# Kernel tuning notes

Measured on AMD Instinct MI355X. Metric: run time of the kernel, lower is better.

Reference implementation:

```python
import jax, jax.numpy as jnp
import numpy as np

TEMPERATURE = 0.1  # init arg `temperature`


def _l2_normalize(x):
    return x / jnp.sqrt(jnp.sum(x * x, axis=1, keepdims=True))


def setup_inputs() -> dict:
    key = jax.random.key(0)
    k1, k2, k3 = jax.random.split(key, 3)
    B, D, Q = 2048, 128, 65536
    projections_1 = jax.random.normal(k1, (B, D), dtype=jnp.float32)
    projections_2 = jax.random.normal(k2, (B, D), dtype=jnp.float32)
    # queue is initialized row-l2-normalized in the original module
    feature_queue = _l2_normalize(jax.random.normal(k3, (Q, D), dtype=jnp.float32))
    return {"projections_1": projections_1, "projections_2": projections_2,
            "feature_queue": feature_queue}


def reference(projections_1, projections_2, feature_queue):
    # NNCLR.contrastive_loss (per-sample losses), including nearest_neighbour.
    p1 = _l2_normalize(projections_1)  # [B, D]
    p2 = _l2_normalize(projections_2)  # [B, D]

    def nearest_neighbour(p):
        # [B, Q] similarity -> top-1 index -> gather from queue
        sims = jnp.einsum('bd,qd->bq', p, feature_queue)
        idx = jnp.argmax(sims, axis=1)  # [B]
        nn = feature_queue[idx]         # [B, D]
        # straight-through: value = nn, gradient flows to p
        return p + jax.lax.stop_gradient(nn - p)

    nn1 = nearest_neighbour(p1)
    nn2 = nearest_neighbour(p2)

    s_1_2_1 = jnp.einsum('id,jd->ij', nn1, p2) / TEMPERATURE
    s_1_2_2 = jnp.einsum('id,jd->ij', p2, nn1) / TEMPERATURE
    s_2_1_1 = jnp.einsum('id,jd->ij', nn2, p1) / TEMPERATURE
    s_2_1_2 = jnp.einsum('id,jd->ij', p1, nn2) / TEMPERATURE

    logits = jnp.concatenate([s_1_2_1, s_1_2_2, s_2_1_1, s_2_1_2], axis=0)  # [4B, B]
    B = p1.shape[0]
    labels = jnp.tile(jnp.arange(B), 4)  # [4B]
    logp = jax.nn.log_softmax(logits, axis=1)
    loss = -jnp.take_along_axis(logp, labels[:, None], axis=1)[:, 0]  # [4B]
    return loss
```

## Files before the change

### kernel.cpp

```cpp
#include <hip/hip_runtime.h>

#define S 132
#define SCALE 10.0f
#define EPS_MARGIN 0.008f
#define SROWS_CAP 480
#define ROWCHUNK 48

typedef __attribute__((ext_vector_type(8))) short short8;
typedef __attribute__((ext_vector_type(4))) float floatx4;

#define MFMA16(a, b, c) __builtin_amdgcn_mfma_f32_16x16x32_bf16((a), (b), (c), 0, 0, 0)

__device__ __forceinline__ unsigned int ordered_bits(float f) {
    unsigned int b = __float_as_uint(f);
    return (b & 0x80000000u) ? ~b : (b | 0x80000000u);
}
__device__ __forceinline__ float from_ordered(unsigned int u) {
    return __uint_as_float((u & 0x80000000u) ? (u ^ 0x80000000u) : ~u);
}
__device__ __forceinline__ short bf_rne(float x) {
    unsigned int u = __float_as_uint(x);
    return (short)((u + 0x7FFFu + ((u >> 16) & 1u)) >> 16);
}
__device__ __forceinline__ float bf2f(short s) {
    return __uint_as_float(((unsigned int)(unsigned short)s) << 16);
}

__global__ __launch_bounds__(256) void k_prep_qcvt(const float* __restrict__ p1,
                                                   const float* __restrict__ p2,
                                                   const float* __restrict__ queue,
                                                   float* __restrict__ pn,
                                                   short* __restrict__ pnb,
                                                   short* __restrict__ qb,
                                                   unsigned int* __restrict__ mbest,
                                                   unsigned long long* __restrict__ best,
                                                   float* __restrict__ sums) {
    int b = blockIdx.x;
    if (b < 1024) {
        int sub = threadIdx.x >> 6;
        int t = threadIdx.x & 63;
        int row = b * 4 + sub;
        const float* src = (row < 2048) ? (p1 + (size_t)row * 128)
                                        : (p2 + (size_t)(row - 2048) * 128);
        float2 v = ((const float2*)src)[t];
        float ss = v.x * v.x + v.y * v.y;
        #pragma unroll
        for (int o = 32; o; o >>= 1) ss += __shfl_xor(ss, o);
        float inv = 1.0f / sqrtf(ss);
        float2 o2; o2.x = v.x * inv; o2.y = v.y * inv;
        ((float2*)(pn + (size_t)row * 128))[t] = o2;
        unsigned int pk = (unsigned int)(unsigned short)bf_rne(o2.x)
                        | ((unsigned int)(unsigned short)bf_rne(o2.y) << 16);
        ((unsigned int*)(pnb + (size_t)row * 128))[t] = pk;
        if (t == 0) { mbest[row] = 0u; best[row] = 0ULL; }
        if (row < 128) sums[row * 64 + t] = 0.0f;
    } else {
        size_t i = ((size_t)(b - 1024) * 256 + threadIdx.x) * 8;
        float4 f0 = *(const float4*)(queue + i);
        float4 f1 = *(const float4*)(queue + i + 4);
        short8 o;
        o[0] = bf_rne(f0.x); o[1] = bf_rne(f0.y); o[2] = bf_rne(f0.z); o[3] = bf_rne(f0.w);
        o[4] = bf_rne(f1.x); o[5] = bf_rne(f1.y); o[6] = bf_rne(f1.z); o[7] = bf_rne(f1.w);
        *(short8*)(qb + i) = o;
    }
}

__device__ __forceinline__ void screen_tile(const short8 A[8][4],
                                            short8 b0, short8 b1, short8 b2, short8 b3,
                                            float rmax[8][4]) {
    floatx4 acc[8];
    floatx4 zero = {0.0f, 0.0f, 0.0f, 0.0f};
    #pragma unroll
    for (int rf = 0; rf < 8; ++rf) acc[rf] = MFMA16(A[rf][0], b0, zero);
    #pragma unroll
    for (int rf = 0; rf < 8; ++rf) acc[rf] = MFMA16(A[rf][1], b1, acc[rf]);
    #pragma unroll
    for (int rf = 0; rf < 8; ++rf) acc[rf] = MFMA16(A[rf][2], b2, acc[rf]);
    #pragma unroll
    for (int rf = 0; rf < 8; ++rf) acc[rf] = MFMA16(A[rf][3], b3, acc[rf]);
    #pragma unroll
    for (int rf = 0; rf < 8; ++rf)
        #pragma unroll
        for (int r = 0; r < 4; ++r) rmax[rf][r] = fmaxf(rmax[rf][r], acc[rf][r]);
}

__global__ __launch_bounds__(256, 2) void k_screen(const short* __restrict__ pnb,
                                                   const short* __restrict__ qb,
                                                   unsigned int* __restrict__ mbest,
                                                   float* __restrict__ smax) {
    int tid = threadIdx.x;
    int lane = tid & 63, wv = tid >> 6;
    int n16 = lane & 15, quad = lane >> 4;

    int id = blockIdx.x;
    int xcd = id & 7;
    int g = id >> 3;
    int rowblk = g & 7;
    int qsub = g >> 3;
    int qsplit = xcd * 8 + qsub;
    int rowbase = rowblk * 512 + wv * 128;
    int qstart = qsplit * 1024;

    short8 A[8][4];
    #pragma unroll
    for (int rf = 0; rf < 8; ++rf) {
        const short* ap = pnb + (size_t)(rowbase + rf * 16 + n16) * 128 + quad * 8;
        #pragma unroll
        for (int kk = 0; kk < 4; ++kk)
            A[rf][kk] = *(const short8*)(ap + kk * 32);
    }
    #pragma unroll
    for (int rf = 0; rf < 8; ++rf)
        #pragma unroll
        for (int kk = 0; kk < 4; ++kk)
            asm volatile("" : "+v"(A[rf][kk]));

    float rmax[8][4];
    #pragma unroll
    for (int rf = 0; rf < 8; ++rf)
        #pragma unroll
        for (int r = 0; r < 4; ++r) rmax[rf][r] = -1e30f;

    const short* lp = qb + (size_t)(qstart + n16) * 128 + quad * 8;
    short8 a0 = *(const short8*)(lp), a1 = *(const short8*)(lp + 32),
           a2 = *(const short8*)(lp + 64), a3 = *(const short8*)(lp + 96);

    for (int t = 0; t < 64; t += 2) {
        if ((t & 15) == 0) __syncthreads();
        const short* p1p = lp + 2048;
        short8 b0 = *(const short8*)(p1p), b1 = *(const short8*)(p1p + 32),
               b2 = *(const short8*)(p1p + 64), b3 = *(const short8*)(p1p + 96);
        screen_tile(A, a0, a1, a2, a3, rmax);
        const short* p2p = lp + 4096;
        a0 = *(const short8*)(p2p); a1 = *(const short8*)(p2p + 32);
        a2 = *(const short8*)(p2p + 64); a3 = *(const short8*)(p2p + 96);
        screen_tile(A, b0, b1, b2, b3, rmax);
        lp += 4096;
    }

    #pragma unroll
    for (int rf = 0; rf < 8; ++rf)
        #pragma unroll
        for (int r = 0; r < 4; ++r) {
            float v = rmax[rf][r];
            v = fmaxf(v, __shfl_xor(v, 1));
            v = fmaxf(v, __shfl_xor(v, 2));
            v = fmaxf(v, __shfl_xor(v, 4));
            v = fmaxf(v, __shfl_xor(v, 8));
            if (n16 == 0) {
                int row = rowbase + rf * 16 + quad * 4 + r;
                atomicMax(&mbest[row], ordered_bits(v));
                smax[(size_t)qsplit * 4096 + row] = v;
            }
        }
}

__global__ __launch_bounds__(256, 4) void k_rescreen(const short* __restrict__ pnb,
                                                     const short* __restrict__ qb,
                                                     const unsigned int* __restrict__ mbest,
                                                     const float* __restrict__ smax,
                                                     const float* __restrict__ pn,
                                                     const float* __restrict__ queue,
                                                     unsigned long long* __restrict__ best) {
    __shared__ unsigned short rows[SROWS_CAP];
    __shared__ int nsh;
    int b = blockIdx.x;
    int s = b & 63;
    int qp = b >> 6;
    int tid = threadIdx.x;
    if (tid == 0) nsh = 0;
    __syncthreads();
    const float* sm = smax + (size_t)s * 4096;
    #pragma unroll
    for (int j = 0; j < 16; ++j) {
        int row = tid + 256 * j;
        float thr = from_ordered(mbest[row]) - EPS_MARGIN;
        if (sm[row] > thr) {
            int pos = atomicAdd(&nsh, 1);
            if (pos < SROWS_CAP) rows[pos] = (unsigned short)row;
        }
    }
    __syncthreads();
    int n = nsh; if (n > SROWS_CAP) n = SROWS_CAP;
    if (n == 0) return;

    int lane = tid & 63, wv = tid >> 6;
    int n16 = lane & 15, quad = lane >> 4;
    int qt = qp * 4 + wv;
    int qrow = s * 1024 + qt * 16 + n16;

    const short* bp = qb + (size_t)qrow * 128 + quad * 8;
    short8 b0 = *(const short8*)(bp);
    short8 b1 = *(const short8*)(bp + 32);
    short8 b2 = *(const short8*)(bp + 64);
    short8 b3 = *(const short8*)(bp + 96);

    for (int base = 0; base < n; base += ROWCHUNK) {
        short8 Af[3][4]; float th[3][4]; int rowC[3][4];
        #pragma unroll
        for (int rt = 0; rt < 3; ++rt) {
            int ia = base + rt * 16 + n16;
            int rA = rows[ia < n ? ia : base];
            const short* ap = pnb + (size_t)rA * 128 + quad * 8;
            #pragma unroll
            for (int kk = 0; kk < 4; ++kk) Af[rt][kk] = *(const short8*)(ap + kk * 32);
            #pragma unroll
            for (int r = 0; r < 4; ++r) {
                int ic = base + rt * 16 + quad * 4 + r;
                if (ic < n) {
                    int rr = rows[ic];
                    rowC[rt][r] = rr;
                    th[rt][r] = from_ordered(mbest[rr]) - EPS_MARGIN;
                } else { rowC[rt][r] = 0; th[rt][r] = 3.0e38f; }
            }
        }
        #pragma unroll
        for (int rt = 0; rt < 3; ++rt) {
            floatx4 zero = {0.0f, 0.0f, 0.0f, 0.0f};
            floatx4 acc = MFMA16(Af[rt][0], b0, zero);
            acc = MFMA16(Af[rt][1], b1, acc);
            acc = MFMA16(Af[rt][2], b2, acc);
            acc = MFMA16(Af[rt][3], b3, acc);
            #pragma unroll
            for (int r = 0; r < 4; ++r) {
                unsigned long long mb = __ballot(acc[r] > th[rt][r]);
                while (mb) {
                    int L = __builtin_ctzll(mb);
                    mb &= mb - 1;
                    int row = __shfl(rowC[rt][r], L);
                    int q   = __shfl(qrow, L);
                    float2 a  = ((const float2*)(pn + (size_t)row * 128))[lane];
                    float2 bq = ((const float2*)(queue + (size_t)q * 128))[lane];
                    float d = a.x * bq.x + a.y * bq.y;
                    #pragma unroll
                    for (int o = 32; o; o >>= 1) d += __shfl_xor(d, o);
                    if (lane == 0) {
                        unsigned long long pk = ((unsigned long long)ordered_bits(d) << 32)
                                              | (unsigned long long)(unsigned int)(~q);
                        atomicMax(&best[row], pk);
                    }
                }
            }
        }
    }
}

__global__ __launch_bounds__(256) void k_gemm_lse(const unsigned long long* __restrict__ best,
                                                  const float* __restrict__ queue,
                                                  const float* __restrict__ pn,
                                                  float* __restrict__ sums,
                                                  float* __restrict__ dg) {
    __shared__ __align__(16) float al[64 * S];
    __shared__ __align__(16) float bl[64 * S];
    __shared__ float red[64][17];
    int tid = threadIdx.x;
    int z = blockIdx.z;
    const float* B = pn + (z ? 0 : 2048 * 128);
    float* rowsum = sums + z * 4096;
    float* colsum = sums + z * 4096 + 2048;
    float* diag = dg + z * 2048;
    int arow0 = z * 2048 + blockIdx.x * 64;

    #pragma unroll
    for (int i = tid; i < 1024; i += 256) {
        int r = i >> 4, c = (i & 15) * 8;
        unsigned int idx = (~(unsigned int)(best[arow0 + r] & 0xFFFFFFFFull)) & 0xFFFFu;
        const float* qr = queue + (size_t)idx * 128 + c;
        float4 f0 = *(const float4*)(qr);
        float4 f1 = *(const float4*)(qr + 4);
        float* dst = &al[r * S + c];
        dst[0] = bf2f(bf_rne(f0.x)); dst[1] = bf2f(bf_rne(f0.y));
        dst[2] = bf2f(bf_rne(f0.z)); dst[3] = bf2f(bf_rne(f0.w));
        dst[4] = bf2f(bf_rne(f1.x)); dst[5] = bf2f(bf_rne(f1.y));
        dst[6] = bf2f(bf_rne(f1.z)); dst[7] = bf2f(bf_rne(f1.w));
    }
    const float4* bsrc = (const float4*)(B + (size_t)blockIdx.y * 64 * 128);
    #pragma unroll
    for (int i = tid; i < 2048; i += 256) {
        int r = i >> 5, c = i & 31;
        *(float4*)&bl[r * S + c * 4] = bsrc[i];
    }
    __syncthreads();
    int ty = tid >> 4, tx = tid & 15;
    float acc[4][4] = {};
    #pragma unroll 2
    for (int k = 0; k < 128; k += 4) {
        float4 a[4], b[4];
        #pragma unroll
        for (int i = 0; i < 4; ++i) a[i] = *(const float4*)&al[(ty + 16 * i) * S + k];
        #pragma unroll
        for (int j = 0; j < 4; ++j) b[j] = *(const float4*)&bl[(tx + 16 * j) * S + k];
        #pragma unroll
        for (int i = 0; i < 4; ++i)
            #pragma unroll
            for (int j = 0; j < 4; ++j)
                acc[i][j] += a[i].x * b[j].x + a[i].y * b[j].y +
                             a[i].z * b[j].z + a[i].w * b[j].w;
    }
    int rowbase = blockIdx.x * 64, colbase = blockIdx.y * 64;

    float e[4][4], rs[4], cs[4];
    #pragma unroll
    for (int i = 0; i < 4; ++i) { rs[i] = 0.0f; cs[i] = 0.0f; }
    #pragma unroll
    for (int i = 0; i < 4; ++i)
        #pragma unroll
        for (int j = 0; j < 4; ++j) {
            e[i][j] = __expf(acc[i][j] * SCALE - 10.0f);
            rs[i] += e[i][j];
        }
    #pragma unroll
    for (int j = 0; j < 4; ++j)
        #pragma unroll
        for (int i = 0; i < 4; ++i) cs[j] += e[i][j];

    if (rowbase == colbase && ty == tx) {
        #pragma unroll
        for (int i = 0; i < 4; ++i) diag[rowbase + ty + 16 * i] = acc[i][i];
    }

    #pragma unroll
    for (int i = 0; i < 4; ++i) red[ty + 16 * i][tx] = rs[i];
    __syncthreads();
    if (tid < 64) {
        float s = 0.0f;
        #pragma unroll
        for (int x = 0; x < 16; ++x) s += red[tid][x];
        atomicAdd(&rowsum[rowbase + tid], s);
    }
    __syncthreads();
    #pragma unroll
    for (int j = 0; j < 4; ++j) red[tx + 16 * j][ty] = cs[j];
    __syncthreads();
    if (tid < 64) {
        float s = 0.0f;
        #pragma unroll
        for (int x = 0; x < 16; ++x) s += red[tid][x];
        atomicAdd(&colsum[colbase + tid], s);
    }
}

__global__ void k_final(const float* __restrict__ sums,
                        const float* __restrict__ dg1, const float* __restrict__ dg2,
                        float* __restrict__ out) {
    int idx = blockIdx.x * 256 + threadIdx.x;
    int seg = idx >> 11, r = idx & 2047;
    float s = sums[seg * 2048 + r];
    float d = (seg < 2) ? dg1[r] : dg2[r];
    out[idx] = 10.0f + logf(s) - d * SCALE;
}

extern "C" void kernel_launch(void* const* d_in, const int* in_sizes, int n_in,
                              void* d_out, int out_size, void* d_ws, size_t ws_size,
                              hipStream_t stream) {
    const float* p1    = (const float*)d_in[0];
    const float* p2    = (const float*)d_in[1];
    const float* queue = (const float*)d_in[2];
    float* out = (float*)d_out;

    char* w = (char*)d_ws;
    float* pn   = (float*)w;
    float* smax = (float*)(w + (2u << 20));
    short* qb   = (short*)(w + (3u << 20));
    short* pnb  = (short*)(w + (19u << 20));
    char* b2 = w + (20u << 20);
    unsigned int* mbest = (unsigned int*)b2;
    unsigned long long* best = (unsigned long long*)(b2 + (16u << 10));
    float* sums = (float*)(b2 + (48u << 10));
    float* dg1  = sums + 8192;
    float* dg2  = dg1 + 2048;

    k_prep_qcvt<<<5120, 256, 0, stream>>>(p1, p2, queue, pn, pnb, qb, mbest, best, sums);
    k_screen<<<512, 256, 0, stream>>>(pnb, qb, mbest, smax);
    k_rescreen<<<64 * 16, 256, 0, stream>>>(pnb, qb, mbest, smax, pn, queue, best);
    k_gemm_lse<<<dim3(32, 32, 2), 256, 0, stream>>>(best, queue, pn, sums, dg1);
    k_final<<<32, 256, 0, stream>>>(sums, dg1, dg2, out);
}
```

Before: 234.8 us.

## Restructure screen kernel with smaller per-wave row tile and software-pipelined MFMA/max

The screening kernel now runs 512-thread blocks where each wave holds 64 query rows instead of 128, and each block covers a 2048-entry queue slice instead of 1024, halving the number of splits. The inner loop is software-pipelined: the MFMA chain for one tile overlaps with the max-reduction of the previous tile's accumulators and with loading the next B fragments. Rescreen indexing is updated to the 32-split layout. Lower register pressure should raise occupancy, but each wave reuses its queue loads over fewer rows, and rescreen candidate counts per split may grow.

Result: slower. 288.0 us (+22.6%).

```diff
diff --git a/kernel.cpp b/kernel.cpp
--- a/kernel.cpp
+++ b/kernel.cpp
@@ -65,26 +65,30 @@
     }
 }
 
-__device__ __forceinline__ void screen_tile(const short8 A[8][4],
-                                            short8 b0, short8 b1, short8 b2, short8 b3,
-                                            float rmax[8][4]) {
-    floatx4 acc[8];
+__device__ __forceinline__ void loadB4(short8 B[4], const short* p) {
+    #pragma unroll
+    for (int kk = 0; kk < 4; ++kk) B[kk] = *(const short8*)(p + kk * 32);
+}
+__device__ __forceinline__ void chain4(const short8 A[4][4], const short8 B[4],
+                                       floatx4 acc[4]) {
     floatx4 zero = {0.0f, 0.0f, 0.0f, 0.0f};
     #pragma unroll
-    for (int rf = 0; rf < 8; ++rf) acc[rf] = MFMA16(A[rf][0], b0, zero);
-    #pragma unroll
-    for (int rf = 0; rf < 8; ++rf) acc[rf] = MFMA16(A[rf][1], b1, acc[rf]);
-    #pragma unroll
-    for (int rf = 0; rf < 8; ++rf) acc[rf] = MFMA16(A[rf][2], b2, acc[rf]);
-    #pragma unroll
-    for (int rf = 0; rf < 8; ++rf) acc[rf] = MFMA16(A[rf][3], b3, acc[rf]);
-    #pragma unroll
-    for (int rf = 0; rf < 8; ++rf)
+    for (int rf = 0; rf < 4; ++rf) acc[rf] = MFMA16(A[rf][0], B[0], zero);
+    #pragma unroll
+    for (int rf = 0; rf < 4; ++rf) acc[rf] = MFMA16(A[rf][1], B[1], acc[rf]);
+    #pragma unroll
+    for (int rf = 0; rf < 4; ++rf) acc[rf] = MFMA16(A[rf][2], B[2], acc[rf]);
+    #pragma unroll
+    for (int rf = 0; rf < 4; ++rf) acc[rf] = MFMA16(A[rf][3], B[3], acc[rf]);
+}
+__device__ __forceinline__ void fmax4(float rmax[4][4], const floatx4 acc[4]) {
+    #pragma unroll
+    for (int rf = 0; rf < 4; ++rf)
         #pragma unroll
         for (int r = 0; r < 4; ++r) rmax[rf][r] = fmaxf(rmax[rf][r], acc[rf][r]);
 }
 
-__global__ __launch_bounds__(256, 2) void k_screen(const short* __restrict__ pnb,
+__global__ __launch_bounds__(512, 2) void k_screen(const short* __restrict__ pnb,
                                                    const short* __restrict__ qb,
                                                    unsigned int* __restrict__ mbest,
                                                    float* __restrict__ smax) {
@@ -97,49 +101,48 @@
     int g = id >> 3;
     int rowblk = g & 7;
     int qsub = g >> 3;
-    int qsplit = xcd * 8 + qsub;
-    int rowbase = rowblk * 512 + wv * 128;
-    int qstart = qsplit * 1024;
-
-    short8 A[8][4];
-    #pragma unroll
-    for (int rf = 0; rf < 8; ++rf) {
+    int qsplit = xcd * 4 + qsub;
+    int rowbase = rowblk * 512 + wv * 64;
+    int qstart = qsplit * 2048;
+
+    short8 A[4][4];
+    #pragma unroll
+    for (int rf = 0; rf < 4; ++rf) {
         const short* ap = pnb + (size_t)(rowbase + rf * 16 + n16) * 128 + quad * 8;
         #pragma unroll
         for (int kk = 0; kk < 4; ++kk)
             A[rf][kk] = *(const short8*)(ap + kk * 32);
     }
-    #pragma unroll
-    for (int rf = 0; rf < 8; ++rf)
-        #pragma unroll
-        for (int kk = 0; kk < 4; ++kk)
-            asm volatile("" : "+v"(A[rf][kk]));
-
-    float rmax[8][4];
-    #pragma unroll
-    for (int rf = 0; rf < 8; ++rf)
+
+    float rmax[4][4];
+    #pragma unroll
+    for (int rf = 0; rf < 4; ++rf)
         #pragma unroll
         for (int r = 0; r < 4; ++r) rmax[rf][r] = -1e30f;
 
     const short* lp = qb + (size_t)(qstart + n16) * 128 + quad * 8;
-    short8 a0 = *(const short8*)(lp), a1 = *(const short8*)(lp + 32),
-           a2 = *(const short8*)(lp + 64), a3 = *(const short8*)(lp + 96);
-
-    for (int t = 0; t < 64; t += 2) {
-        if ((t & 15) == 0) __syncthreads();
-        const short* p1p = lp + 2048;
-        short8 b0 = *(const short8*)(p1p), b1 = *(const short8*)(p1p + 32),
-               b2 = *(const short8*)(p1p + 64), b3 = *(const short8*)(p1p + 96);
-        screen_tile(A, a0, a1, a2, a3, rmax);
-        const short* p2p = lp + 4096;
-        a0 = *(const short8*)(p2p); a1 = *(const short8*)(p2p + 32);
-        a2 = *(const short8*)(p2p + 64); a3 = *(const short8*)(p2p + 96);
-        screen_tile(A, b0, b1, b2, b3, rmax);
-        lp += 4096;
-    }
-
-    #pragma unroll
-    for (int rf = 0; rf < 8; ++rf)
+    short8 Ba[4], Bb[4];
+    floatx4 accA[4], accB[4];
+
+    loadB4(Ba, lp);
+    chain4(A, Ba, accB);
+    loadB4(Bb, lp + 2048);
+
+    for (int t = 1; t < 127; t += 2) {
+        if (((t - 1) & 15) == 0) __syncthreads();
+        loadB4(Ba, lp + (size_t)(t + 1) * 2048);
+        chain4(A, Bb, accA);
+        fmax4(rmax, accB);
+        loadB4(Bb, lp + (size_t)(t + 2) * 2048);
+        chain4(A, Ba, accB);
+        fmax4(rmax, accA);
+    }
+    chain4(A, Bb, accA);
+    fmax4(rmax, accB);
+    fmax4(rmax, accA);
+
+    #pragma unroll
+    for (int rf = 0; rf < 4; ++rf)
         #pragma unroll
         for (int r = 0; r < 4; ++r) {
             float v = rmax[rf][r];
@@ -165,8 +168,8 @@
     __shared__ unsigned short rows[SROWS_CAP];
     __shared__ int nsh;
     int b = blockIdx.x;
-    int s = b & 63;
-    int qp = b >> 6;
+    int s = b & 31;
+    int qp = b >> 5;
     int tid = threadIdx.x;
     if (tid == 0) nsh = 0;
     __syncthreads();
@@ -187,7 +190,7 @@
     int lane = tid & 63, wv = tid >> 6;
     int n16 = lane & 15, quad = lane >> 4;
     int qt = qp * 4 + wv;
-    int qrow = s * 1024 + qt * 16 + n16;
+    int qrow = s * 2048 + qt * 16 + n16;
 
     const short* bp = qb + (size_t)qrow * 128 + quad * 8;
     short8 b0 = *(const short8*)(bp);
@@ -371,8 +374,8 @@
     float* dg2  = dg1 + 2048;
 
     k_prep_qcvt<<<5120, 256, 0, stream>>>(p1, p2, queue, pn, pnb, qb, mbest, best, sums);
-    k_screen<<<512, 256, 0, stream>>>(pnb, qb, mbest, smax);
-    k_rescreen<<<64 * 16, 256, 0, stream>>>(pnb, qb, mbest, smax, pn, queue, best);
+    k_screen<<<256, 512, 0, stream>>>(pnb, qb, mbest, smax);
+    k_rescreen<<<32 * 32, 256, 0, stream>>>(pnb, qb, mbest, smax, pn, queue, best);
     k_gemm_lse<<<dim3(32, 32, 2), 256, 0, stream>>>(best, queue, pn, sums, dg1);
     k_final<<<32, 256, 0, stream>>>(sums, dg1, dg2, out);
 }
```

## Run the logits GEMM on bf16 MFMA with a hi/lo split of the projections

Applied to the files above, without the earlier changes.

Replaces the fp32 LDS-tiled FMA GEMM in k_gemm_lse with bf16 MFMA 16x16x32 instructions. The normalized projections are split into high and low bf16 parts in the prep kernel to keep near-fp32 accuracy on the B operand, while the nearest-neighbour rows stay bf16-rounded as before. Tiles grow to 128x128 with operands loaded straight into registers instead of through shared memory, and row and column sums are reduced with shuffles. The cost is an extra bf16 buffer written in prep and twice as many MFMAs for the hi/lo passes, but it removes the scalar FMA bottleneck.

Measured after the change: 215.5 us. 1.09x faster.

```diff
diff --git a/kernel.cpp b/kernel.cpp
--- a/kernel.cpp
+++ b/kernel.cpp
@@ -1,6 +1,5 @@
 #include <hip/hip_runtime.h>
 
-#define S 132
 #define SCALE 10.0f
 #define EPS_MARGIN 0.008f
 #define SROWS_CAP 480
@@ -31,6 +30,7 @@
                                                    const float* __restrict__ queue,
                                                    float* __restrict__ pn,
                                                    short* __restrict__ pnb,
+                                                   short* __restrict__ pnl,
                                                    short* __restrict__ qb,
                                                    unsigned int* __restrict__ mbest,
                                                    unsigned long long* __restrict__ best,
@@ -49,9 +49,14 @@
         float inv = 1.0f / sqrtf(ss);
         float2 o2; o2.x = v.x * inv; o2.y = v.y * inv;
         ((float2*)(pn + (size_t)row * 128))[t] = o2;
-        unsigned int pk = (unsigned int)(unsigned short)bf_rne(o2.x)
-                        | ((unsigned int)(unsigned short)bf_rne(o2.y) << 16);
+        short hx = bf_rne(o2.x), hy = bf_rne(o2.y);
+        unsigned int pk = (unsigned int)(unsigned short)hx
+                        | ((unsigned int)(unsigned short)hy << 16);
         ((unsigned int*)(pnb + (size_t)row * 128))[t] = pk;
+        short lx = bf_rne(o2.x - bf2f(hx)), ly = bf_rne(o2.y - bf2f(hy));
+        unsigned int pl = (unsigned int)(unsigned short)lx
+                        | ((unsigned int)(unsigned short)ly << 16);
+        ((unsigned int*)(pnl + (size_t)row * 128))[t] = pl;
         if (t == 0) { mbest[row] = 0u; best[row] = 0ULL; }
         if (row < 128) sums[row * 64 + t] = 0.0f;
     } else {
@@ -245,98 +250,97 @@
     }
 }
 
-__global__ __launch_bounds__(256) void k_gemm_lse(const unsigned long long* __restrict__ best,
-                                                  const float* __restrict__ queue,
-                                                  const float* __restrict__ pn,
-                                                  float* __restrict__ sums,
-                                                  float* __restrict__ dg) {
-    __shared__ __align__(16) float al[64 * S];
-    __shared__ __align__(16) float bl[64 * S];
-    __shared__ float red[64][17];
+__global__ __launch_bounds__(256, 2) void k_gemm_lse(const unsigned long long* __restrict__ best,
+                                                     const float* __restrict__ queue,
+                                                     const short* __restrict__ pnb,
+                                                     const short* __restrict__ pnl,
+                                                     float* __restrict__ sums,
+                                                     float* __restrict__ dg) {
+    __shared__ float red[4][128];
     int tid = threadIdx.x;
-    int z = blockIdx.z;
-    const float* B = pn + (z ? 0 : 2048 * 128);
+    int lane = tid & 63, wv = tid >> 6;
+    int n16 = lane & 15, quad = lane >> 4;
+    int z = blockIdx.z, xb = blockIdx.x, yb = blockIdx.y;
+
+    short8 A[2][4];
+    #pragma unroll
+    for (int rf = 0; rf < 2; ++rf) {
+        int row = z * 2048 + xb * 128 + wv * 32 + rf * 16 + n16;
+        unsigned int idx = (~(unsigned int)(best[row] & 0xFFFFFFFFull)) & 0xFFFFu;
+        const float* qr = queue + (size_t)idx * 128 + quad * 8;
+        #pragma unroll
+        for (int kk = 0; kk < 4; ++kk) {
+            float4 f0 = *(const float4*)(qr + kk * 32);
+            float4 f1 = *(const float4*)(qr + kk * 32 + 4);
+            short8 a;
+            a[0] = bf_rne(f0.x); a[1] = bf_rne(f0.y); a[2] = bf_rne(f0.z); a[3] = bf_rne(f0.w);
+            a[4] = bf_rne(f1.x); a[5] = bf_rne(f1.y); a[6] = bf_rne(f1.z); a[7] = bf_rne(f1.w);
+            A[rf][kk] = a;
+        }
+    }
+
+    int bbase = (z ? 0 : 2048) + yb * 128;
+    const short* bh0 = pnb + (size_t)(bbase + n16) * 128 + quad * 8;
+    const short* bl0 = pnl + (size_t)(bbase + n16) * 128 + quad * 8;
+
+    float rs[2][4] = {};
     float* rowsum = sums + z * 4096;
     float* colsum = sums + z * 4096 + 2048;
-    float* diag = dg + z * 2048;
-    int arow0 = z * 2048 + blockIdx.x * 64;
-
-    #pragma unroll
-    for (int i = tid; i < 1024; i += 256) {
-        int r = i >> 4, c = (i & 15) * 8;
-        unsigned int idx = (~(unsigned int)(best[arow0 + r] & 0xFFFFFFFFull)) & 0xFFFFu;
-        const float* qr = queue + (size_t)idx * 128 + c;
-        float4 f0 = *(const float4*)(qr);
-        float4 f1 = *(const float4*)(qr + 4);
-        float* dst = &al[r * S + c];
-        dst[0] = bf2f(bf_rne(f0.x)); dst[1] = bf2f(bf_rne(f0.y));
-        dst[2] = bf2f(bf_rne(f0.z)); dst[3] = bf2f(bf_rne(f0.w));
-        dst[4] = bf2f(bf_rne(f1.x)); dst[5] = bf2f(bf_rne(f1.y));
-        dst[6] = bf2f(bf_rne(f1.z)); dst[7] = bf2f(bf_rne(f1.w));
-    }
-    const float4* bsrc = (const float4*)(B + (size_t)blockIdx.y * 64 * 128);
-    #pragma unroll
-    for (int i = tid; i < 2048; i += 256) {
-        int r = i >> 5, c = i & 31;
-        *(float4*)&bl[r * S + c * 4] = bsrc[i];
-    }
+
+    #pragma unroll 1
+    for (int ct = 0; ct < 8; ++ct) {
+        const short* ph = bh0 + (size_t)ct * 16 * 128;
+        const short* pl = bl0 + (size_t)ct * 16 * 128;
+        short8 h0 = *(const short8*)(ph),      h1 = *(const short8*)(ph + 32),
+               h2 = *(const short8*)(ph + 64), h3 = *(const short8*)(ph + 96);
+        short8 l0 = *(const short8*)(pl),      l1 = *(const short8*)(pl + 32),
+               l2 = *(const short8*)(pl + 64), l3 = *(const short8*)(pl + 96);
+        floatx4 acc0, acc1;
+        floatx4 zero = {0.0f, 0.0f, 0.0f, 0.0f};
+        acc0 = MFMA16(A[0][0], h0, zero); acc1 = MFMA16(A[1][0], h0, zero);
+        acc0 = MFMA16(A[0][1], h1, acc0); acc1 = MFMA16(A[1][1], h1, acc1);
+        acc0 = MFMA16(A[0][2], h2, acc0); acc1 = MFMA16(A[1][2], h2, acc1);
+        acc0 = MFMA16(A[0][3], h3, acc0); acc1 = MFMA16(A[1][3], h3, acc1);
+        acc0 = MFMA16(A[0][0], l0, acc0); acc1 = MFMA16(A[1][0], l0, acc1);
+        acc0 = MFMA16(A[0][1], l1, acc0); acc1 = MFMA16(A[1][1], l1, acc1);
+        acc0 = MFMA16(A[0][2], l2, acc0); acc1 = MFMA16(A[1][2], l2, acc1);
+        acc0 = MFMA16(A[0][3], l3, acc0); acc1 = MFMA16(A[1][3], l3, acc1);
+
+        float csv = 0.0f;
+        #pragma unroll
+        for (int rf = 0; rf < 2; ++rf)
+            #pragma unroll
+            for (int r = 0; r < 4; ++r) {
+                float a = rf ? acc1[r] : acc0[r];
+                int row_l = wv * 32 + rf * 16 + quad * 4 + r;
+                if (xb == yb && row_l == ct * 16 + n16)
+                    dg[z * 2048 + xb * 128 + row_l] = a;
+                float e = __expf(a * SCALE - 10.0f);
+                rs[rf][r] += e;
+                csv += e;
+            }
+        csv += __shfl_xor(csv, 16);
+        csv += __shfl_xor(csv, 32);
+        if (quad == 0) red[wv][ct * 16 + n16] = csv;
+    }
+
+    #pragma unroll
+    for (int rf = 0; rf < 2; ++rf)
+        #pragma unroll
+        for (int r = 0; r < 4; ++r) {
+            float v = rs[rf][r];
+            v += __shfl_xor(v, 1);
+            v += __shfl_xor(v, 2);
+            v += __shfl_xor(v, 4);
+            v += __shfl_xor(v, 8);
+            if (n16 == 0)
+                atomicAdd(&rowsum[xb * 128 + wv * 32 + rf * 16 + quad * 4 + r], v);
+        }
+
     __syncthreads();
-    int ty = tid >> 4, tx = tid & 15;
-    float acc[4][4] = {};
-    #pragma unroll 2
-    for (int k = 0; k < 128; k += 4) {
-        float4 a[4], b[4];
-        #pragma unroll
-        for (int i = 0; i < 4; ++i) a[i] = *(const float4*)&al[(ty + 16 * i) * S + k];
-        #pragma unroll
-        for (int j = 0; j < 4; ++j) b[j] = *(const float4*)&bl[(tx + 16 * j) * S + k];
-        #pragma unroll
-        for (int i = 0; i < 4; ++i)
-            #pragma unroll
-            for (int j = 0; j < 4; ++j)
-                acc[i][j] += a[i].x * b[j].x + a[i].y * b[j].y +
-                             a[i].z * b[j].z + a[i].w * b[j].w;
-    }
-    int rowbase = blockIdx.x * 64, colbase = blockIdx.y * 64;
-
-    float e[4][4], rs[4], cs[4];
-    #pragma unroll
-    for (int i = 0; i < 4; ++i) { rs[i] = 0.0f; cs[i] = 0.0f; }
-    #pragma unroll
-    for (int i = 0; i < 4; ++i)
-        #pragma unroll
-        for (int j = 0; j < 4; ++j) {
-            e[i][j] = __expf(acc[i][j] * SCALE - 10.0f);
-            rs[i] += e[i][j];
-        }
-    #pragma unroll
-    for (int j = 0; j < 4; ++j)
-        #pragma unroll
-        for (int i = 0; i < 4; ++i) cs[j] += e[i][j];
-
-    if (rowbase == colbase && ty == tx) {
-        #pragma unroll
-        for (int i = 0; i < 4; ++i) diag[rowbase + ty + 16 * i] = acc[i][i];
-    }
-
-    #pragma unroll
-    for (int i = 0; i < 4; ++i) red[ty + 16 * i][tx] = rs[i];
-    __syncthreads();
-    if (tid < 64) {
-        float s = 0.0f;
-        #pragma unroll
-        for (int x = 0; x < 16; ++x) s += red[tid][x];
-        atomicAdd(&rowsum[rowbase + tid], s);
-    }
-    __syncthreads();
-    #pragma unroll
-    for (int j = 0; j < 4; ++j) red[tx + 16 * j][ty] = cs[j];
-    __syncthreads();
-    if (tid < 64) {
-        float s = 0.0f;
-        #pragma unroll
-        for (int x = 0; x < 16; ++x) s += red[tid][x];
-        atomicAdd(&colsum[colbase + tid], s);
+    if (tid < 128) {
+        float s = red[0][tid] + red[1][tid] + red[2][tid] + red[3][tid];
+        atomicAdd(&colsum[yb * 128 + tid], s);
     }
 }
 
@@ -363,16 +367,17 @@
     float* smax = (float*)(w + (2u << 20));
     short* qb   = (short*)(w + (3u << 20));
     short* pnb  = (short*)(w + (19u << 20));
-    char* b2 = w + (20u << 20);
+    short* pnl  = (short*)(w + (20u << 20));
+    char* b2 = w + (21u << 20);
     unsigned int* mbest = (unsigned int*)b2;
     unsigned long long* best = (unsigned long long*)(b2 + (16u << 10));
     float* sums = (float*)(b2 + (48u << 10));
     float* dg1  = sums + 8192;
     float* dg2  = dg1 + 2048;
 
-    k_prep_qcvt<<<5120, 256, 0, stream>>>(p1, p2, queue, pn, pnb, qb, mbest, best, sums);
+    k_prep_qcvt<<<5120, 256, 0, stream>>>(p1, p2, queue, pn, pnb, pnl, qb, mbest, best, sums);
     k_screen<<<512, 256, 0, stream>>>(pnb, qb, mbest, smax);
     k_rescreen<<<64 * 16, 256, 0, stream>>>(pnb, qb, mbest, smax, pn, queue, best);
-    k_gemm_lse<<<dim3(32, 32, 2), 256, 0, stream>>>(best, queue, pn, sums, dg1);
+    k_gemm_lse<<<dim3(16, 16, 2), 256, 0, stream>>>(best, queue, pnb, pnl, sums, dg1);
     k_final<<<32, 256, 0, stream>>>(sums, dg1, dg2, out);
 }
```
